# Optimization experiments

Measured on AMD Instinct MI355X. Metric: run time of the kernel, lower is better.

The kernel has to match this reference:

```python
import jax, jax.numpy as jnp
import numpy as np

B, N, K, C_IN, M, C_OUT = 2, 20000, 16, 128, 9, 128


def setup_inputs() -> dict:
    key = jax.random.key(0)
    k1, k2, k3, k4, k5, k6 = jax.random.split(key, 6)
    x = jax.random.normal(k1, (B, N, C_IN), dtype=jnp.float32)
    # 0 == "no neighbor" (maps to the prepended zero row); valid ids are 1..N
    adj = jax.random.randint(k2, (N, K), 0, N, dtype=jnp.int32)
    W = jax.random.uniform(k3, (M, C_OUT, C_IN), jnp.float32, -0.05, 0.05)
    b = jax.random.uniform(k4, (C_OUT,), jnp.float32, -0.05, 0.05)
    u = jax.random.uniform(k5, (M, C_IN), jnp.float32, -0.05, 0.05)
    c = jax.random.uniform(k6, (M,), jnp.float32, -0.05, 0.05)
    return {"x": x, "adj": adj, "W": W, "b": b, "u": u, "c": c}


def reference(x, adj, W, b, u, c):
    Bb, Nn, Cin = x.shape
    # prepend zero row so adj==0 gathers zeros (padding neighbor)
    xp = jnp.concatenate([jnp.zeros((Bb, 1, Cin), x.dtype), x], axis=1)
    patches = xp[:, adj]                      # [B, N, K, C] neighbor features
    # pseudo-coordinate differences -> soft assignment over M kernels
    diff = x[:, :, None, :] - patches          # [B, N, K, C]
    logits = jnp.einsum('bnkc,mc->bnkm', diff, u) + c
    q = jax.nn.softmax(logits, axis=-1)        # softmax over M (last axis)
    # inverse neighbor count (0 where the node has no neighbors)
    deg = jnp.count_nonzero(adj, axis=1).astype(x.dtype)        # [N]
    deg_inv = jnp.where(deg > 0, 1.0 / jnp.maximum(deg, 1.0), 0.0)
    # out[b,n,o] = deg_inv[n] * sum_{k,m} q[b,n,k,m] * (W[m] @ x_nbr)[o]
    msg = jnp.einsum('bnkm,moc,bnkc->bno', q, W, patches)        # [B, N, O]
    return msg * deg_inv[None, :, None] + b
```

## Files before the change

kernel.cpp:

```cpp
#include <hip/hip_runtime.h>
#include <hip/hip_bf16.h>

#define NB 2
#define NN 20000
#define NKN 16
#define NC 128
#define NM 9
#define NO 128
#define NR (NB*NN)
#define KK (NM*NC)
#define NKC (KK/32)
#define NPB 16
#define YS 12
#define QS (NKN*12+4)
#define YB (NR/64)

typedef short bf16x8 __attribute__((ext_vector_type(8)));
typedef float f32x4 __attribute__((ext_vector_type(4)));
typedef float f32x2 __attribute__((ext_vector_type(2)));
typedef unsigned short u16x8 __attribute__((ext_vector_type(8)));

__device__ inline f32x2 bfpair(unsigned int w) {
    union { unsigned int u; float f; } lo, hi;
    lo.u = w << 16; hi.u = w & 0xFFFF0000u;
    return (f32x2){lo.f, hi.f};
}

__global__ __launch_bounds__(256) void prep_kernel(const float* __restrict__ x,
                                                   const float* __restrict__ u,
                                                   const float* __restrict__ W,
                                                   float* __restrict__ y,
                                                   __hip_bfloat16* __restrict__ xb,
                                                   __hip_bfloat16* __restrict__ Wg,
                                                   int use_xb) {
    int tid = threadIdx.x;
    if (blockIdx.x < YB) {
        int wave = tid >> 6, lane = tid & 63;
        int lr = lane & 15, quad = lane >> 4;
        int node0 = blockIdx.x * 64 + wave * 16;
        long xbase = (long)(node0 + lr) * NC;

        bf16x8 afr[4];
        #pragma unroll
        for (int kc = 0; kc < 4; kc++) {
            const float* px = x + xbase + kc * 32 + quad * 8;
            float4 a0 = *(const float4*)px;
            float4 a1 = *(const float4*)(px + 4);
            union { bf16x8 v; unsigned short s[8]; __hip_bfloat16 h[8]; } af;
            af.h[0] = __float2bfloat16(a0.x); af.h[1] = __float2bfloat16(a0.y);
            af.h[2] = __float2bfloat16(a0.z); af.h[3] = __float2bfloat16(a0.w);
            af.h[4] = __float2bfloat16(a1.x); af.h[5] = __float2bfloat16(a1.y);
            af.h[6] = __float2bfloat16(a1.z); af.h[7] = __float2bfloat16(a1.w);
            afr[kc] = af.v;
            if (use_xb)
                *(u16x8*)((unsigned short*)xb + xbase + kc * 32 + quad * 8) =
                    *(u16x8*)&af.v;
        }
        int cs = (lr < NM) ? lr : 0;
        float fz = (lr < NM) ? 1.f : 0.f;
        f32x4 acc = (f32x4){0.f, 0.f, 0.f, 0.f};
        #pragma unroll
        for (int kc = 0; kc < 4; kc++) {
            const float* pu = u + cs * NC + kc * 32 + quad * 8;
            float4 b0 = *(const float4*)pu;
            float4 b1 = *(const float4*)(pu + 4);
            union { bf16x8 v; __hip_bfloat16 h[8]; } bf;
            bf.h[0] = __float2bfloat16(b0.x * fz); bf.h[1] = __float2bfloat16(b0.y * fz);
            bf.h[2] = __float2bfloat16(b0.z * fz); bf.h[3] = __float2bfloat16(b0.w * fz);
            bf.h[4] = __float2bfloat16(b1.x * fz); bf.h[5] = __float2bfloat16(b1.y * fz);
            bf.h[6] = __float2bfloat16(b1.z * fz); bf.h[7] = __float2bfloat16(b1.w * fz);
            acc = __builtin_amdgcn_mfma_f32_16x16x32_bf16(afr[kc], bf.v, acc, 0, 0, 0);
        }
        if (lr < NM) {
            #pragma unroll
            for (int r = 0; r < 4; r++)
                y[(long)(node0 + quad * 4 + r) * YS + lr] = acc[r];
        }
    } else {
        int t = (blockIdx.x - YB) * 256 + tid;
        int kk = t >> 7;
        int o = t & 127;
        int m = kk >> 7;
        int c = kk & 127;
        float v = W[m * 16384 + o * 128 + c];
        Wg[((kk >> 5) * 128 + o) * 32 + (kk & 31)] = __float2bfloat16(v);
    }
}

template<bool BF16G>
__global__ __launch_bounds__(256, 4) void fused_kernel(const float* __restrict__ x,
                                                       const __hip_bfloat16* __restrict__ xb,
                                                       const int* __restrict__ adj,
                                                       const float* __restrict__ y,
                                                       const float* __restrict__ cv,
                                                       const __hip_bfloat16* __restrict__ Wg,
                                                       const float* __restrict__ bv,
                                                       float* __restrict__ out) {
    __shared__ __align__(16) short s_S[NPB * KK];
    int*   s_adj = (int*)s_S;
    float* s_q   = (float*)((char*)s_S + 1024);

    int tid = threadIdx.x;
    int node0 = blockIdx.x * NPB;
    int b = node0 / NN;
    int n0 = node0 - b * NN;
    int ln = tid >> 4, k = tid & 15;

    int a = adj[(n0 + ln) * NKN + k];
    const float* yn = y + (long)(node0 + ln) * YS;
    const float* ya = y + (long)(b * NN + ((a > 0) ? a - 1 : 0)) * YS;
    float4 yn0 = *(const float4*)yn;
    float4 yn1 = *(const float4*)(yn + 4);
    float  yn8 = yn[8];
    float4 ya0 = *(const float4*)ya;
    float4 ya1 = *(const float4*)(ya + 4);
    float  ya8 = ya[8];
    s_adj[ln * NKN + k] = a;
    __syncthreads();

    int c8 = k << 3;
    int idx[NKN]; int d = 0;
    #pragma unroll
    for (int j = 0; j < NKN; j++) {
        int aa = s_adj[ln * NKN + j];
        d += (aa > 0);
        idx[j] = (aa > 0) ? aa - 1 : 0;
    }
    float di = (d > 0) ? 1.f / (float)d : 0.f;

    uint4 pw0[8];
    if (BF16G) {
        #pragma unroll
        for (int j = 0; j < 8; j++)
            pw0[j] = *(const uint4*)((const unsigned short*)xb +
                                     (long)(b * NN + idx[j]) * NC + c8);
    }

    {
        float sel = (a > 0) ? 1.f : 0.f;
        float l[NM];
        l[0] = yn0.x - sel * ya0.x + cv[0];
        l[1] = yn0.y - sel * ya0.y + cv[1];
        l[2] = yn0.z - sel * ya0.z + cv[2];
        l[3] = yn0.w - sel * ya0.w + cv[3];
        l[4] = yn1.x - sel * ya1.x + cv[4];
        l[5] = yn1.y - sel * ya1.y + cv[5];
        l[6] = yn1.z - sel * ya1.z + cv[6];
        l[7] = yn1.w - sel * ya1.w + cv[7];
        l[8] = yn8   - sel * ya8   + cv[8];
        float mx = l[0];
        #pragma unroll
        for (int m = 1; m < NM; m++) mx = fmaxf(mx, l[m]);
        float e[NM]; float sum = 0.f;
        #pragma unroll
        for (int m = 0; m < NM; m++) { e[m] = expf(l[m] - mx); sum += e[m]; }
        float qs = (a > 0) ? (1.f / sum) : 0.f;
        #pragma unroll
        for (int m = 0; m < NM; m++) s_q[ln * QS + k * 12 + m] = e[m] * qs;
    }
    __syncthreads();

    f32x2 s2[NM][4];
    #pragma unroll
    for (int m = 0; m < NM; m++)
        #pragma unroll
        for (int j = 0; j < 4; j++) s2[m][j] = (f32x2){0.f, 0.f};

    #define ACC_ALL(P0, P1, P2, P3, KK2) {                                    \
        const float* qr = &s_q[ln * QS + (KK2) * 12];                         \
        float4 qa = *(const float4*)qr;                                       \
        float4 qb = *(const float4*)(qr + 4);                                 \
        float  q8 = qr[8];                                                    \
        f32x2 qq;                                                             \
        qq=(f32x2){qa.x,qa.x}; s2[0][0]+=qq*P0; s2[0][1]+=qq*P1; s2[0][2]+=qq*P2; s2[0][3]+=qq*P3; \
        qq=(f32x2){qa.y,qa.y}; s2[1][0]+=qq*P0; s2[1][1]+=qq*P1; s2[1][2]+=qq*P2; s2[1][3]+=qq*P3; \
        qq=(f32x2){qa.z,qa.z}; s2[2][0]+=qq*P0; s2[2][1]+=qq*P1; s2[2][2]+=qq*P2; s2[2][3]+=qq*P3; \
        qq=(f32x2){qa.w,qa.w}; s2[3][0]+=qq*P0; s2[3][1]+=qq*P1; s2[3][2]+=qq*P2; s2[3][3]+=qq*P3; \
        qq=(f32x2){qb.x,qb.x}; s2[4][0]+=qq*P0; s2[4][1]+=qq*P1; s2[4][2]+=qq*P2; s2[4][3]+=qq*P3; \
        qq=(f32x2){qb.y,qb.y}; s2[5][0]+=qq*P0; s2[5][1]+=qq*P1; s2[5][2]+=qq*P2; s2[5][3]+=qq*P3; \
        qq=(f32x2){qb.z,qb.z}; s2[6][0]+=qq*P0; s2[6][1]+=qq*P1; s2[6][2]+=qq*P2; s2[6][3]+=qq*P3; \
        qq=(f32x2){qb.w,qb.w}; s2[7][0]+=qq*P0; s2[7][1]+=qq*P1; s2[7][2]+=qq*P2; s2[7][3]+=qq*P3; \
        qq=(f32x2){q8,q8};     s2[8][0]+=qq*P0; s2[8][1]+=qq*P1; s2[8][2]+=qq*P2; s2[8][3]+=qq*P3; }

    if (BF16G) {
        uint4 pw1[8];
        #pragma unroll
        for (int j = 0; j < 8; j++)
            pw1[j] = *(const uint4*)((const unsigned short*)xb +
                                     (long)(b * NN + idx[8 + j]) * NC + c8);
        #pragma unroll
        for (int j = 0; j < 8; j++) {
            f32x2 p0 = bfpair(pw0[j].x), p1 = bfpair(pw0[j].y);
            f32x2 p2 = bfpair(pw0[j].z), p3 = bfpair(pw0[j].w);
            ACC_ALL(p0, p1, p2, p3, j)
        }
        #pragma unroll
        for (int j = 0; j < 8; j++) {
            f32x2 p0 = bfpair(pw1[j].x), p1 = bfpair(pw1[j].y);
            f32x2 p2 = bfpair(pw1[j].z), p3 = bfpair(pw1[j].w);
            ACC_ALL(p0, p1, p2, p3, 8 + j)
        }
    } else {
        #pragma unroll
        for (int g = 0; g < NKN / 4; g++) {
            float4 fa[4], fb[4];
            #pragma unroll
            for (int j = 0; j < 4; j++) {
                const float* px = x + (long)(b * NN + idx[g * 4 + j]) * NC + c8;
                fa[j] = *(const float4*)px;
                fb[j] = *(const float4*)(px + 4);
            }
            #pragma unroll
            for (int j = 0; j < 4; j++) {
                f32x2 p0 = (f32x2){fa[j].x, fa[j].y}, p1 = (f32x2){fa[j].z, fa[j].w};
                f32x2 p2 = (f32x2){fb[j].x, fb[j].y}, p3 = (f32x2){fb[j].z, fb[j].w};
                ACC_ALL(p0, p1, p2, p3, g * 4 + j)
            }
        }
    }
    #undef ACC_ALL
    __syncthreads();

    #pragma unroll
    for (int m = 0; m < NM; m++) {
        u16x8 ov;
        #pragma unroll
        for (int j = 0; j < 4; j++) {
            union { unsigned short h; __hip_bfloat16 bb; } c0, c1;
            c0.bb = __float2bfloat16(s2[m][j][0] * di);
            c1.bb = __float2bfloat16(s2[m][j][1] * di);
            ov[j * 2]     = c0.h;
            ov[j * 2 + 1] = c1.h;
        }
        int g = m * 16 + k;
        int gs = g ^ (ln & 7);
        *(u16x8*)(&s_S[ln * KK + gs * 8]) = ov;
    }
    __syncthreads();

    int wave = tid >> 6;
    int lane = tid & 63;
    int lr = lane & 15;
    int quad = lane >> 4;
    const short* wg = reinterpret_cast<const short*>(Wg);
    f32x4 acc0 = (f32x4){0.f,0.f,0.f,0.f};
    f32x4 acc1 = (f32x4){0.f,0.f,0.f,0.f};
    int ct0 = wave * 2;

    #pragma unroll 9
    for (int kc = 0; kc < NKC; kc++) {
        int g = kc * 4 + quad;
        int gs = g ^ (lr & 7);
        bf16x8 afrag = *(const bf16x8*)(&s_S[lr * KK + gs * 8]);
        bf16x8 b0 = *(const bf16x8*)(wg + ((kc * 128) + ct0 * 16 + lr) * 32 + quad * 8);
        bf16x8 b1 = *(const bf16x8*)(wg + ((kc * 128) + (ct0 + 1) * 16 + lr) * 32 + quad * 8);
        acc0 = __builtin_amdgcn_mfma_f32_16x16x32_bf16(afrag, b0, acc0, 0, 0, 0);
        acc1 = __builtin_amdgcn_mfma_f32_16x16x32_bf16(afrag, b1, acc1, 0, 0, 0);
    }

    int col0 = ct0 * 16 + lr;
    int col1 = col0 + 16;
    float bb0 = bv[col0];
    float bb1 = bv[col1];
    int rbase = node0 + quad * 4;
    #pragma unroll
    for (int r = 0; r < 4; r++) {
        out[(long)(rbase + r) * NO + col0] = acc0[r] + bb0;
        out[(long)(rbase + r) * NO + col1] = acc1[r] + bb1;
    }
}

extern "C" void kernel_launch(void* const* d_in, const int* in_sizes, int n_in,
                              void* d_out, int out_size, void* d_ws, size_t ws_size,
                              hipStream_t stream) {
    const float* x   = (const float*)d_in[0];
    const int*   adj = (const int*)  d_in[1];
    const float* W   = (const float*)d_in[2];
    const float* bv  = (const float*)d_in[3];
    const float* u   = (const float*)d_in[4];
    const float* cv  = (const float*)d_in[5];
    float* out = (float*)d_out;

    char* ws = (char*)d_ws;
    float* y = (float*)ws;
    __hip_bfloat16* Wg = (__hip_bfloat16*)(ws + 1920000);
    __hip_bfloat16* xb = (__hip_bfloat16*)(ws + 2214912);
    bool use_xb = (ws_size >= (size_t)12454912);

    prep_kernel<<<YB + 576, 256, 0, stream>>>(x, u, W, y, use_xb ? xb : nullptr, Wg,
                                              use_xb ? 1 : 0);
    if (use_xb)
        fused_kernel<true><<<NR / NPB, 256, 0, stream>>>(x, xb, adj, y, cv, Wg, bv, out);
    else
        fused_kernel<false><<<NR / NPB, 256, 0, stream>>>(x, xb, adj, y, cv, Wg, bv, out);
}
```

Baseline: 145.0 us.

## Double threads per block, splitting channels and output tiles per thread

The fused kernel now launches 512 threads per block instead of 256. Each (node, neighbor) pair is handled by two threads that each gather 4 channels rather than 8, so per-thread accumulators drop from 9x4 to 9x2 float pairs. In the MFMA stage each of the 8 waves computes one 16-column output tile instead of two. The aim is more parallelism and lower register pressure to hide gather latency, at the cost of redundant softmax/adj work per thread pair and smaller per-thread loads.

After: 157.6 us. 8.7% more time.

```diff
diff --git a/kernel.cpp b/kernel.cpp
--- a/kernel.cpp
+++ b/kernel.cpp
@@ -19,6 +19,7 @@
 typedef float f32x4 __attribute__((ext_vector_type(4)));
 typedef float f32x2 __attribute__((ext_vector_type(2)));
 typedef unsigned short u16x8 __attribute__((ext_vector_type(8)));
+typedef unsigned short u16x4 __attribute__((ext_vector_type(4)));
 
 __device__ inline f32x2 bfpair(unsigned int w) {
     union { unsigned int u; float f; } lo, hi;
@@ -88,14 +89,16 @@
 }
 
 template<bool BF16G>
-__global__ __launch_bounds__(256, 4) void fused_kernel(const float* __restrict__ x,
-                                                       const __hip_bfloat16* __restrict__ xb,
-                                                       const int* __restrict__ adj,
-                                                       const float* __restrict__ y,
-                                                       const float* __restrict__ cv,
-                                                       const __hip_bfloat16* __restrict__ Wg,
-                                                       const float* __restrict__ bv,
-                                                       float* __restrict__ out) {
+__global__ __launch_bounds__(512)
+__attribute__((amdgpu_waves_per_eu(4, 4)))
+void fused_kernel(const float* __restrict__ x,
+                  const __hip_bfloat16* __restrict__ xb,
+                  const int* __restrict__ adj,
+                  const float* __restrict__ y,
+                  const float* __restrict__ cv,
+                  const __hip_bfloat16* __restrict__ Wg,
+                  const float* __restrict__ bv,
+                  float* __restrict__ out) {
     __shared__ __align__(16) short s_S[NPB * KK];
     int*   s_adj = (int*)s_S;
     float* s_q   = (float*)((char*)s_S + 1024);
@@ -104,7 +107,9 @@
     int node0 = blockIdx.x * NPB;
     int b = node0 / NN;
     int n0 = node0 - b * NN;
-    int ln = tid >> 4, k = tid & 15;
+    int ln = tid >> 5;
+    int k  = (tid >> 1) & 15;
+    int h  = tid & 1;
 
     int a = adj[(n0 + ln) * NKN + k];
     const float* yn = y + (long)(node0 + ln) * YS;
@@ -115,10 +120,10 @@
     float4 ya0 = *(const float4*)ya;
     float4 ya1 = *(const float4*)(ya + 4);
     float  ya8 = ya[8];
-    s_adj[ln * NKN + k] = a;
-    __syncthreads();
-
-    int c8 = k << 3;
+    if (h == 0) s_adj[ln * NKN + k] = a;
+    __syncthreads();
+
+    int c4 = (2 * k + h) * 4;
     int idx[NKN]; int d = 0;
     #pragma unroll
     for (int j = 0; j < NKN; j++) {
@@ -128,12 +133,12 @@
     }
     float di = (d > 0) ? 1.f / (float)d : 0.f;
 
-    uint4 pw0[8];
+    uint2 pw[NKN];
     if (BF16G) {
         #pragma unroll
-        for (int j = 0; j < 8; j++)
-            pw0[j] = *(const uint4*)((const unsigned short*)xb +
-                                     (long)(b * NN + idx[j]) * NC + c8);
+        for (int j = 0; j < NKN; j++)
+            pw[j] = *(const uint2*)((const unsigned short*)xb +
+                                    (long)(b * NN + idx[j]) * NC + c4);
     }
 
     {
@@ -155,67 +160,48 @@
         #pragma unroll
         for (int m = 0; m < NM; m++) { e[m] = expf(l[m] - mx); sum += e[m]; }
         float qs = (a > 0) ? (1.f / sum) : 0.f;
-        #pragma unroll
-        for (int m = 0; m < NM; m++) s_q[ln * QS + k * 12 + m] = e[m] * qs;
-    }
-    __syncthreads();
-
-    f32x2 s2[NM][4];
-    #pragma unroll
-    for (int m = 0; m < NM; m++)
-        #pragma unroll
-        for (int j = 0; j < 4; j++) s2[m][j] = (f32x2){0.f, 0.f};
-
-    #define ACC_ALL(P0, P1, P2, P3, KK2) {                                    \
-        const float* qr = &s_q[ln * QS + (KK2) * 12];                         \
+        if (h == 0) {
+            #pragma unroll
+            for (int m = 0; m < NM; m++) s_q[ln * QS + k * 12 + m] = e[m] * qs;
+        }
+    }
+    __syncthreads();
+
+    f32x2 s2[NM][2];
+    #pragma unroll
+    for (int m = 0; m < NM; m++) {
+        s2[m][0] = (f32x2){0.f, 0.f};
+        s2[m][1] = (f32x2){0.f, 0.f};
+    }
+
+    #define ACC_ALL(P0, P1, J) {                                              \
+        const float* qr = &s_q[ln * QS + (J) * 12];                           \
         float4 qa = *(const float4*)qr;                                       \
         float4 qb = *(const float4*)(qr + 4);                                 \
         float  q8 = qr[8];                                                    \
         f32x2 qq;                                                             \
-        qq=(f32x2){qa.x,qa.x}; s2[0][0]+=qq*P0; s2[0][1]+=qq*P1; s2[0][2]+=qq*P2; s2[0][3]+=qq*P3; \
-        qq=(f32x2){qa.y,qa.y}; s2[1][0]+=qq*P0; s2[1][1]+=qq*P1; s2[1][2]+=qq*P2; s2[1][3]+=qq*P3; \
-        qq=(f32x2){qa.z,qa.z}; s2[2][0]+=qq*P0; s2[2][1]+=qq*P1; s2[2][2]+=qq*P2; s2[2][3]+=qq*P3; \
-        qq=(f32x2){qa.w,qa.w}; s2[3][0]+=qq*P0; s2[3][1]+=qq*P1; s2[3][2]+=qq*P2; s2[3][3]+=qq*P3; \
-        qq=(f32x2){qb.x,qb.x}; s2[4][0]+=qq*P0; s2[4][1]+=qq*P1; s2[4][2]+=qq*P2; s2[4][3]+=qq*P3; \
-        qq=(f32x2){qb.y,qb.y}; s2[5][0]+=qq*P0; s2[5][1]+=qq*P1; s2[5][2]+=qq*P2; s2[5][3]+=qq*P3; \
-        qq=(f32x2){qb.z,qb.z}; s2[6][0]+=qq*P0; s2[6][1]+=qq*P1; s2[6][2]+=qq*P2; s2[6][3]+=qq*P3; \
-        qq=(f32x2){qb.w,qb.w}; s2[7][0]+=qq*P0; s2[7][1]+=qq*P1; s2[7][2]+=qq*P2; s2[7][3]+=qq*P3; \
-        qq=(f32x2){q8,q8};     s2[8][0]+=qq*P0; s2[8][1]+=qq*P1; s2[8][2]+=qq*P2; s2[8][3]+=qq*P3; }
+        qq=(f32x2){qa.x,qa.x}; s2[0][0]+=qq*P0; s2[0][1]+=qq*P1;              \
+        qq=(f32x2){qa.y,qa.y}; s2[1][0]+=qq*P0; s2[1][1]+=qq*P1;              \
+        qq=(f32x2){qa.z,qa.z}; s2[2][0]+=qq*P0; s2[2][1]+=qq*P1;              \
+        qq=(f32x2){qa.w,qa.w}; s2[3][0]+=qq*P0; s2[3][1]+=qq*P1;              \
+        qq=(f32x2){qb.x,qb.x}; s2[4][0]+=qq*P0; s2[4][1]+=qq*P1;              \
+        qq=(f32x2){qb.y,qb.y}; s2[5][0]+=qq*P0; s2[5][1]+=qq*P1;              \
+        qq=(f32x2){qb.z,qb.z}; s2[6][0]+=qq*P0; s2[6][1]+=qq*P1;              \
+        qq=(f32x2){qb.w,qb.w}; s2[7][0]+=qq*P0; s2[7][1]+=qq*P1;              \
+        qq=(f32x2){q8,q8};     s2[8][0]+=qq*P0; s2[8][1]+=qq*P1; }
 
     if (BF16G) {
-        uint4 pw1[8];
-        #pragma unroll
-        for (int j = 0; j < 8; j++)
-            pw1[j] = *(const uint4*)((const unsigned short*)xb +
-                                     (long)(b * NN + idx[8 + j]) * NC + c8);
-        #pragma unroll
-        for (int j = 0; j < 8; j++) {
-            f32x2 p0 = bfpair(pw0[j].x), p1 = bfpair(pw0[j].y);
-            f32x2 p2 = bfpair(pw0[j].z), p3 = bfpair(pw0[j].w);
-            ACC_ALL(p0, p1, p2, p3, j)
-        }
-        #pragma unroll
-        for (int j = 0; j < 8; j++) {
-            f32x2 p0 = bfpair(pw1[j].x), p1 = bfpair(pw1[j].y);
-            f32x2 p2 = bfpair(pw1[j].z), p3 = bfpair(pw1[j].w);
-            ACC_ALL(p0, p1, p2, p3, 8 + j)
+        #pragma unroll
+        for (int j = 0; j < NKN; j++) {
+            f32x2 p0 = bfpair(pw[j].x), p1 = bfpair(pw[j].y);
+            ACC_ALL(p0, p1, j)
         }
     } else {
         #pragma unroll
-        for (int g = 0; g < NKN / 4; g++) {
-            float4 fa[4], fb[4];
-            #pragma unroll
-            for (int j = 0; j < 4; j++) {
-                const float* px = x + (long)(b * NN + idx[g * 4 + j]) * NC + c8;
-                fa[j] = *(const float4*)px;
-                fb[j] = *(const float4*)(px + 4);
-            }
-            #pragma unroll
-            for (int j = 0; j < 4; j++) {
-                f32x2 p0 = (f32x2){fa[j].x, fa[j].y}, p1 = (f32x2){fa[j].z, fa[j].w};
-                f32x2 p2 = (f32x2){fb[j].x, fb[j].y}, p3 = (f32x2){fb[j].z, fb[j].w};
-                ACC_ALL(p0, p1, p2, p3, g * 4 + j)
-            }
+        for (int j = 0; j < NKN; j++) {
+            float4 fa = *(const float4*)(x + (long)(b * NN + idx[j]) * NC + c4);
+            f32x2 p0 = (f32x2){fa.x, fa.y}, p1 = (f32x2){fa.z, fa.w};
+            ACC_ALL(p0, p1, j)
         }
     }
     #undef ACC_ALL
@@ -223,18 +209,16 @@
 
     #pragma unroll
     for (int m = 0; m < NM; m++) {
-        u16x8 ov;
-        #pragma unroll
-        for (int j = 0; j < 4; j++) {
-            union { unsigned short h; __hip_bfloat16 bb; } c0, c1;
-            c0.bb = __float2bfloat16(s2[m][j][0] * di);
-            c1.bb = __float2bfloat16(s2[m][j][1] * di);
-            ov[j * 2]     = c0.h;
-            ov[j * 2 + 1] = c1.h;
-        }
+        u16x4 ov;
+        union { unsigned short hh; __hip_bfloat16 bb; } c0, c1, c2, c3;
+        c0.bb = __float2bfloat16(s2[m][0][0] * di);
+        c1.bb = __float2bfloat16(s2[m][0][1] * di);
+        c2.bb = __float2bfloat16(s2[m][1][0] * di);
+        c3.bb = __float2bfloat16(s2[m][1][1] * di);
+        ov[0] = c0.hh; ov[1] = c1.hh; ov[2] = c2.hh; ov[3] = c3.hh;
         int g = m * 16 + k;
         int gs = g ^ (ln & 7);
-        *(u16x8*)(&s_S[ln * KK + gs * 8]) = ov;
+        *(u16x4*)(&s_S[ln * KK + gs * 8 + h * 4]) = ov;
     }
     __syncthreads();
 
@@ -243,31 +227,23 @@
     int lr = lane & 15;
     int quad = lane >> 4;
     const short* wg = reinterpret_cast<const short*>(Wg);
-    f32x4 acc0 = (f32x4){0.f,0.f,0.f,0.f};
-    f32x4 acc1 = (f32x4){0.f,0.f,0.f,0.f};
-    int ct0 = wave * 2;
-
-    #pragma unroll 9
+    f32x4 acc = (f32x4){0.f, 0.f, 0.f, 0.f};
+
+    #pragma unroll 12
     for (int kc = 0; kc < NKC; kc++) {
         int g = kc * 4 + quad;
         int gs = g ^ (lr & 7);
         bf16x8 afrag = *(const bf16x8*)(&s_S[lr * KK + gs * 8]);
-        bf16x8 b0 = *(const bf16x8*)(wg + ((kc * 128) + ct0 * 16 + lr) * 32 + quad * 8);
-        bf16x8 b1 = *(const bf16x8*)(wg + ((kc * 128) + (ct0 + 1) * 16 + lr) * 32 + quad * 8);
-        acc0 = __builtin_amdgcn_mfma_f32_16x16x32_bf16(afrag, b0, acc0, 0, 0, 0);
-        acc1 = __builtin_amdgcn_mfma_f32_16x16x32_bf16(afrag, b1, acc1, 0, 0, 0);
-    }
-
-    int col0 = ct0 * 16 + lr;
-    int col1 = col0 + 16;
-    float bb0 = bv[col0];
-    float bb1 = bv[col1];
+        bf16x8 bfrag = *(const bf16x8*)(wg + ((kc * 128) + wave * 16 + lr) * 32 + quad * 8);
+        acc = __builtin_amdgcn_mfma_f32_16x16x32_bf16(afrag, bfrag, acc, 0, 0, 0);
+    }
+
+    int col = wave * 16 + lr;
+    float bb = bv[col];
     int rbase = node0 + quad * 4;
     #pragma unroll
-    for (int r = 0; r < 4; r++) {
-        out[(long)(rbase + r) * NO + col0] = acc0[r] + bb0;
-        out[(long)(rbase + r) * NO + col1] = acc1[r] + bb1;
-    }
+    for (int r = 0; r < 4; r++)
+        out[(long)(rbase + r) * NO + col] = acc[r] + bb;
 }
 
 extern "C" void kernel_launch(void* const* d_in, const int* in_sizes, int n_in,
@@ -290,7 +266,7 @@
     prep_kernel<<<YB + 576, 256, 0, stream>>>(x, u, W, y, use_xb ? xb : nullptr, Wg,
                                               use_xb ? 1 : 0);
     if (use_xb)
-        fused_kernel<true><<<NR / NPB, 256, 0, stream>>>(x, xb, adj, y, cv, Wg, bv, out);
+        fused_kernel<true><<<NR / NPB, 512, 0, stream>>>(x, xb, adj, y, cv, Wg, bv, out);
     else
-        fused_kernel<false><<<NR / NPB, 256, 0, stream>>>(x, xb, adj, y, cv, Wg, bv, out);
-}
+        fused_kernel<false><<<NR / NPB, 512, 0, stream>>>(x, xb, adj, y, cv, Wg, bv, out);
+}
```
